# Kernel tuning notes

Measured on AMD Instinct MI355X. Metric: run time of the kernel, lower is better.

The kernel has to match this reference:

```python
import jax, jax.numpy as jnp
import numpy as np

EPS = 1e-6

def setup_inputs() -> dict:
    key = jax.random.key(0)
    kX, ky, kl, kg, ks, kp = jax.random.split(key, 6)
    B, T, N = 65536, 512, 5000
    X = jax.random.randint(kX, (B, 4), 0, N, dtype=jnp.int32)
    y = jax.random.randint(ky, (B, T), 0, 2, dtype=jnp.int32)
    learn_w = jax.random.normal(kl, (N, 1), dtype=jnp.float32)
    guess_w = jax.random.normal(kg, (N, 1), dtype=jnp.float32)
    slip_w = jax.random.normal(ks, (N, 1), dtype=jnp.float32)
    prior_w = jax.random.normal(kp, (N, 1), dtype=jnp.float32)
    return {"X": X, "y": y, "learn_w": learn_w, "guess_w": guess_w,
            "slip_w": slip_w, "prior_w": prior_w}

def _bkt_forward(X, y, learn_w, guess_w, slip_w, prior_w):
    # per-student BKT parameters, each (B,)
    l = jax.nn.sigmoid(learn_w[X[:, 0], 0])
    g = jax.nn.sigmoid(guess_w[X[:, 1], 0])
    s = jax.nn.sigmoid(slip_w[X[:, 2], 0])
    p = jax.nn.sigmoid(prior_w[X[:, 3], 0])
    y_obs = jnp.where(y == -1, 0, y).astype(l.dtype)  # (B, T), -1 padding -> 0

    def step(latent, y_t):
        # latent: (B,) mastery prob at time t (recorded BEFORE update)
        correct = latent * (1 - s) + (1 - latent) * g
        k_t1 = latent * (1 - s) / correct
        k_t0 = latent * s / (latent * s + (1 - latent) * (1 - g))
        k_t = jnp.where(y_t > 0.5, k_t1, k_t0)
        next_latent = jnp.clip(k_t + (1 - k_t) * l, EPS, 1 - EPS)
        return next_latent, (correct, latent)

    _, (corrects, latents) = jax.lax.scan(step, p, y_obs.T)  # scan over T
    return corrects.T, latents.T  # (B, T) each

def reference(X, y, learn_w, guess_w, slip_w, prior_w):
    return _bkt_forward(X, y, learn_w, guess_w, slip_w, prior_w)
```

## Files before the change

### kernel.cpp

```cpp
#include <hip/hip_runtime.h>
#include <cmath>


#define LSTR 36

typedef float floatx4 __attribute__((ext_vector_type(4)));

__global__ __launch_bounds__(256, 1) void bkt_fwd(
    const int* __restrict__ X,
    const int* __restrict__ Y,
    const float* __restrict__ learn_w,
    const float* __restrict__ guess_w,
    const float* __restrict__ slip_w,
    const float* __restrict__ prior_w,
    float* __restrict__ out,
    int B, int T)
{
#pragma clang fp contract(off)
    const int tid = threadIdx.x;
    const int b = blockIdx.x * 256 + tid;

    __shared__ float xp[256 * LSTR];

    const int4 xi = *reinterpret_cast<const int4*>(X + (size_t)b * 4);
    const float l = (float)(1.0 / (1.0 + exp(-(double)learn_w[xi.x])));
    const float g = (float)(1.0 / (1.0 + exp(-(double)guess_w[xi.y])));
    const float s = (float)(1.0 / (1.0 + exp(-(double)slip_w[xi.z])));
    const float p = (float)(1.0 / (1.0 + exp(-(double)prior_w[xi.w])));

    const float oms = 1.0f - s;
    const float omg = 1.0f - g;
    const float lo  = 1e-6f;
    const float hi  = (float)(1.0 - 1e-6);
    float latent = p;

    const int4* __restrict__ yv = reinterpret_cast<const int4*>(Y + (size_t)b * T);
    unsigned int yp[16];
    #pragma unroll
    for (int w = 0; w < 16; ++w) {
        unsigned int m = 0;
        #pragma unroll
        for (int q = 0; q < 8; ++q) {
            const int4 v = yv[w * 8 + q];
            m |= (v.x > 0 ? 1u : 0u) << (q * 4 + 0);
            m |= (v.y > 0 ? 1u : 0u) << (q * 4 + 1);
            m |= (v.z > 0 ? 1u : 0u) << (q * 4 + 2);
            m |= (v.w > 0 ? 1u : 0u) << (q * 4 + 3);
        }
        yp[w] = m;
    }

    const int wv = tid >> 6, ln = tid & 63;
    const int r8 = ln >> 3, c8 = ln & 7;
    float* __restrict__ lrow = xp + tid * LSTR;
    const float* __restrict__ lrd = xp + (wv * 64 + r8) * LSTR + c8 * 4;
    float* __restrict__ gco = out + (size_t)(blockIdx.x * 256 + wv * 64 + r8) * T + c8 * 4;
    float* __restrict__ gla = gco + (size_t)B * T;

    constexpr int STEPS = 32, NQ = 8;
    const int nOuter = T / STEPS;

    for (int o = 0; o < nOuter; ++o) {
        const unsigned int ycur = yp[0];

        float cr[STEPS], lt[STEPS];
        #pragma unroll
        for (int j = 0; j < STEPS; ++j) {
            const float a       = latent * oms;
            const float omlat   = 1.0f - latent;
            const float t1      = omlat * g;
            const float correct = a + t1;
            const float n0      = latent * s;
            const float t2      = omlat * omg;
            const float d0      = n0 + t2;
            const bool hit = (ycur >> j) & 1u;
            const float num = hit ? a : n0;
            const float den = hit ? correct : d0;
            const float k   = num / den;
            cr[j] = correct;
            lt[j] = latent;
            const float omk = 1.0f - k;
            const float t3  = omk * l;
            const float nxt = k + t3;
            latent = fminf(fmaxf(nxt, lo), hi);
        }

        const int colo = o * STEPS;

        #pragma unroll
        for (int q = 0; q < NQ; ++q)
            *reinterpret_cast<float4*>(lrow + q * 4) =
                make_float4(cr[4*q], cr[4*q+1], cr[4*q+2], cr[4*q+3]);
        __builtin_amdgcn_wave_barrier();
        #pragma unroll
        for (int q = 0; q < NQ; ++q) {
            const floatx4 v = *reinterpret_cast<const floatx4*>(lrd + (q * 8) * LSTR);
            __builtin_nontemporal_store(v,
                reinterpret_cast<floatx4*>(gco + (size_t)(q * 8) * T + colo));
        }
        __builtin_amdgcn_wave_barrier();

        #pragma unroll
        for (int q = 0; q < NQ; ++q)
            *reinterpret_cast<float4*>(lrow + q * 4) =
                make_float4(lt[4*q], lt[4*q+1], lt[4*q+2], lt[4*q+3]);
        __builtin_amdgcn_wave_barrier();
        #pragma unroll
        for (int q = 0; q < NQ; ++q) {
            const floatx4 v = *reinterpret_cast<const floatx4*>(lrd + (q * 8) * LSTR);
            __builtin_nontemporal_store(v,
                reinterpret_cast<floatx4*>(gla + (size_t)(q * 8) * T + colo));
        }
        __builtin_amdgcn_wave_barrier();

        #pragma unroll
        for (int w = 0; w < 15; ++w) yp[w] = yp[w + 1];
    }
}

extern "C" void kernel_launch(void* const* d_in, const int* in_sizes, int n_in,
                              void* d_out, int out_size, void* d_ws, size_t ws_size,
                              hipStream_t stream)
{
    const int*   X  = (const int*)d_in[0];
    const int*   Y  = (const int*)d_in[1];
    const float* lw = (const float*)d_in[2];
    const float* gw = (const float*)d_in[3];
    const float* sw = (const float*)d_in[4];
    const float* pw = (const float*)d_in[5];
    float* out = (float*)d_out;

    const int B = in_sizes[0] / 4;
    const int T = in_sizes[1] / B;

    const int threads = 256;
    const int blocks = B / threads;
    bkt_fwd<<<blocks, threads, 0, stream>>>(X, Y, lw, gw, sw, pw, out, B, T);
}
```

Baseline: 82.74 us.

## Split BKT scan into seed pass and parallel chunked emit pass

A first kernel runs the sequential recurrence per student without storing outputs. It records the latent state at every 32-step boundary plus the packed answer bits and parameters in workspace. A second kernel launches 16 threads per student, each recomputing one 32-step chunk from its seed and writing coalesced rows through swizzled shared memory. This aims to decouple the serial dependency chain from the output write bandwidth and raise occupancy for the store-heavy phase, at the cost of computing the recurrence twice and an extra launch plus workspace traffic.

```diff
diff --git a/kernel.cpp b/kernel.cpp
--- a/kernel.cpp
+++ b/kernel.cpp
@@ -2,25 +2,19 @@
 #include <cmath>
 
 
-#define LSTR 36
-
 typedef float floatx4 __attribute__((ext_vector_type(4)));
 
-__global__ __launch_bounds__(256, 1) void bkt_fwd(
-    const int* __restrict__ X,
-    const int* __restrict__ Y,
-    const float* __restrict__ learn_w,
-    const float* __restrict__ guess_w,
-    const float* __restrict__ slip_w,
-    const float* __restrict__ prior_w,
-    float* __restrict__ out,
+__global__ __launch_bounds__(256, 1) void bkt_seed(
+    const int* __restrict__ X, const int* __restrict__ Y,
+    const float* __restrict__ learn_w, const float* __restrict__ guess_w,
+    const float* __restrict__ slip_w,  const float* __restrict__ prior_w,
+    float* __restrict__ seeds,
+    unsigned int* __restrict__ bits,
+    float* __restrict__ prm,
     int B, int T)
 {
 #pragma clang fp contract(off)
-    const int tid = threadIdx.x;
-    const int b = blockIdx.x * 256 + tid;
-
-    __shared__ float xp[256 * LSTR];
+    const int b = blockIdx.x * 256 + threadIdx.x;
 
     const int4 xi = *reinterpret_cast<const int4*>(X + (size_t)b * 4);
     const float l = (float)(1.0 / (1.0 + exp(-(double)learn_w[xi.x])));
@@ -28,28 +22,186 @@
     const float s = (float)(1.0 / (1.0 + exp(-(double)slip_w[xi.z])));
     const float p = (float)(1.0 / (1.0 + exp(-(double)prior_w[xi.w])));
 
-    const float oms = 1.0f - s;
-    const float omg = 1.0f - g;
-    const float lo  = 1e-6f;
-    const float hi  = (float)(1.0 - 1e-6);
+    const float oms = 1.0f - s, omg = 1.0f - g;
+    const float lo = 1e-6f, hi = (float)(1.0 - 1e-6);
+    float latent = p;
+
+    const int4* __restrict__ yv = reinterpret_cast<const int4*>(Y + (size_t)b * T);
+
+    int4 cur[8], nxt[8];
+    #pragma unroll
+    for (int q = 0; q < 8; ++q) cur[q] = yv[q];
+
+    float sd[16];
+    unsigned int yw[16];
+
+    for (int o = 0; o < 16; ++o) {
+        if (o + 1 < 16) {
+            #pragma unroll
+            for (int q = 0; q < 8; ++q) nxt[q] = yv[(o + 1) * 8 + q];
+        }
+        unsigned int m = 0;
+        #pragma unroll
+        for (int q = 0; q < 8; ++q) {
+            m |= (cur[q].x > 0 ? 1u : 0u) << (q * 4 + 0);
+            m |= (cur[q].y > 0 ? 1u : 0u) << (q * 4 + 1);
+            m |= (cur[q].z > 0 ? 1u : 0u) << (q * 4 + 2);
+            m |= (cur[q].w > 0 ? 1u : 0u) << (q * 4 + 3);
+        }
+        yw[o] = m;
+        sd[o] = latent;
+
+        #pragma unroll
+        for (int j = 0; j < 32; ++j) {
+            const float a       = latent * oms;
+            const float omlat   = 1.0f - latent;
+            const float t1      = omlat * g;
+            const float correct = a + t1;
+            const float n0      = latent * s;
+            const float t2      = omlat * omg;
+            const float d0      = n0 + t2;
+            const bool hit = (m >> j) & 1u;
+            const float num = hit ? a : n0;
+            const float den = hit ? correct : d0;
+            const float k   = num / den;
+            (void)correct;
+            const float omk = 1.0f - k;
+            const float t3  = omk * l;
+            const float nxt2 = k + t3;
+            latent = fminf(fmaxf(nxt2, lo), hi);
+        }
+        #pragma unroll
+        for (int q = 0; q < 8; ++q) cur[q] = nxt[q];
+    }
+
+    #pragma unroll
+    for (int q = 0; q < 4; ++q)
+        *reinterpret_cast<float4*>(seeds + (size_t)b * 16 + q * 4) =
+            make_float4(sd[4*q], sd[4*q+1], sd[4*q+2], sd[4*q+3]);
+    #pragma unroll
+    for (int q = 0; q < 4; ++q)
+        *reinterpret_cast<uint4*>(bits + (size_t)b * 16 + q * 4) =
+            make_uint4(yw[4*q], yw[4*q+1], yw[4*q+2], yw[4*q+3]);
+    *reinterpret_cast<float4*>(prm + (size_t)b * 4) = make_float4(l, g, s, p);
+}
+
+__global__ __launch_bounds__(256) void bkt_emit(
+    const float* __restrict__ seeds, const unsigned int* __restrict__ bits,
+    const float* __restrict__ prm, float* __restrict__ out, int B, int T)
+{
+#pragma clang fp contract(off)
+    const int tid = threadIdx.x;
+    const int stl = tid >> 4;
+    const int ch  = tid & 15;
+    const size_t st = (size_t)blockIdx.x * 16 + stl;
+
+    const float4 pr = *reinterpret_cast<const float4*>(prm + st * 4);
+    const float l = pr.x, g = pr.y, s = pr.z;
+    const float oms = 1.0f - s, omg = 1.0f - g;
+    const float lo = 1e-6f, hi = (float)(1.0 - 1e-6);
+
+    float latent = seeds[st * 16 + ch];
+    const unsigned int m = bits[st * 16 + ch];
+
+    float cr[32], lt[32];
+    #pragma unroll
+    for (int j = 0; j < 32; ++j) {
+        const float a       = latent * oms;
+        const float omlat   = 1.0f - latent;
+        const float t1      = omlat * g;
+        const float correct = a + t1;
+        const float n0      = latent * s;
+        const float t2      = omlat * omg;
+        const float d0      = n0 + t2;
+        const bool hit = (m >> j) & 1u;
+        const float num = hit ? a : n0;
+        const float den = hit ? correct : d0;
+        const float k   = num / den;
+        cr[j] = correct;
+        lt[j] = latent;
+        const float omk = 1.0f - k;
+        const float t3  = omk * l;
+        const float nxt = k + t3;
+        latent = fminf(fmaxf(nxt, lo), hi);
+    }
+
+    __shared__ float xs[16 * 512];
+
+    const int wv = tid >> 6, ln = tid & 63;
+    float* __restrict__ myseg = xs + stl * 512 + ch * 32;
+
+    #pragma unroll
+    for (int q = 0; q < 8; ++q)
+        *reinterpret_cast<float4*>(myseg + ((q ^ (ch & 7)) << 2)) =
+            make_float4(cr[4*q], cr[4*q+1], cr[4*q+2], cr[4*q+3]);
+    __syncthreads();
+    #pragma unroll
+    for (int i = 0; i < 8; ++i) {
+        const int srow = wv * 4 + (i >> 1);
+        const int f4   = (i & 1) * 64 + ln;
+        const int chx  = f4 >> 3, qx = f4 & 7;
+        const floatx4 v = *reinterpret_cast<const floatx4*>(
+            xs + srow * 512 + chx * 32 + ((qx ^ (chx & 7)) << 2));
+        const size_t row = (size_t)blockIdx.x * 16 + srow;
+        __builtin_nontemporal_store(v,
+            reinterpret_cast<floatx4*>(out + row * T + f4 * 4));
+    }
+    __syncthreads();
+
+    #pragma unroll
+    for (int q = 0; q < 8; ++q)
+        *reinterpret_cast<float4*>(myseg + ((q ^ (ch & 7)) << 2)) =
+            make_float4(lt[4*q], lt[4*q+1], lt[4*q+2], lt[4*q+3]);
+    __syncthreads();
+    #pragma unroll
+    for (int i = 0; i < 8; ++i) {
+        const int srow = wv * 4 + (i >> 1);
+        const int f4   = (i & 1) * 64 + ln;
+        const int chx  = f4 >> 3, qx = f4 & 7;
+        const floatx4 v = *reinterpret_cast<const floatx4*>(
+            xs + srow * 512 + chx * 32 + ((qx ^ (chx & 7)) << 2));
+        const size_t row = (size_t)blockIdx.x * 16 + srow;
+        __builtin_nontemporal_store(v,
+            reinterpret_cast<floatx4*>(out + (size_t)B * T + row * T + f4 * 4));
+    }
+}
+
+#define LSTR 36
+__global__ __launch_bounds__(256, 1) void bkt_fwd(
+    const int* __restrict__ X, const int* __restrict__ Y,
+    const float* __restrict__ learn_w, const float* __restrict__ guess_w,
+    const float* __restrict__ slip_w,  const float* __restrict__ prior_w,
+    float* __restrict__ out, int B, int T)
+{
+#pragma clang fp contract(off)
+    const int tid = threadIdx.x;
+    const int b = blockIdx.x * 256 + tid;
+    __shared__ float xp[256 * LSTR];
+
+    const int4 xi = *reinterpret_cast<const int4*>(X + (size_t)b * 4);
+    const float l = (float)(1.0 / (1.0 + exp(-(double)learn_w[xi.x])));
+    const float g = (float)(1.0 / (1.0 + exp(-(double)guess_w[xi.y])));
+    const float s = (float)(1.0 / (1.0 + exp(-(double)slip_w[xi.z])));
+    const float p = (float)(1.0 / (1.0 + exp(-(double)prior_w[xi.w])));
+    const float oms = 1.0f - s, omg = 1.0f - g;
+    const float lo = 1e-6f, hi = (float)(1.0 - 1e-6);
     float latent = p;
 
     const int4* __restrict__ yv = reinterpret_cast<const int4*>(Y + (size_t)b * T);
     unsigned int yp[16];
     #pragma unroll
     for (int w = 0; w < 16; ++w) {
-        unsigned int m = 0;
+        unsigned int mm = 0;
         #pragma unroll
         for (int q = 0; q < 8; ++q) {
             const int4 v = yv[w * 8 + q];
-            m |= (v.x > 0 ? 1u : 0u) << (q * 4 + 0);
-            m |= (v.y > 0 ? 1u : 0u) << (q * 4 + 1);
-            m |= (v.z > 0 ? 1u : 0u) << (q * 4 + 2);
-            m |= (v.w > 0 ? 1u : 0u) << (q * 4 + 3);
-        }
-        yp[w] = m;
-    }
-
+            mm |= (v.x > 0 ? 1u : 0u) << (q * 4 + 0);
+            mm |= (v.y > 0 ? 1u : 0u) << (q * 4 + 1);
+            mm |= (v.z > 0 ? 1u : 0u) << (q * 4 + 2);
+            mm |= (v.w > 0 ? 1u : 0u) << (q * 4 + 3);
+        }
+        yp[w] = mm;
+    }
     const int wv = tid >> 6, ln = tid & 63;
     const int r8 = ln >> 3, c8 = ln & 7;
     float* __restrict__ lrow = xp + tid * LSTR;
@@ -57,15 +209,11 @@
     float* __restrict__ gco = out + (size_t)(blockIdx.x * 256 + wv * 64 + r8) * T + c8 * 4;
     float* __restrict__ gla = gco + (size_t)B * T;
 
-    constexpr int STEPS = 32, NQ = 8;
-    const int nOuter = T / STEPS;
-
-    for (int o = 0; o < nOuter; ++o) {
+    for (int o = 0; o < 16; ++o) {
         const unsigned int ycur = yp[0];
-
-        float cr[STEPS], lt[STEPS];
-        #pragma unroll
-        for (int j = 0; j < STEPS; ++j) {
+        float cr[32], lt[32];
+        #pragma unroll
+        for (int j = 0; j < 32; ++j) {
             const float a       = latent * oms;
             const float omlat   = 1.0f - latent;
             const float t1      = omlat * g;
@@ -77,42 +225,37 @@
             const float num = hit ? a : n0;
             const float den = hit ? correct : d0;
             const float k   = num / den;
-            cr[j] = correct;
-            lt[j] = latent;
+            cr[j] = correct; lt[j] = latent;
             const float omk = 1.0f - k;
             const float t3  = omk * l;
             const float nxt = k + t3;
             latent = fminf(fmaxf(nxt, lo), hi);
         }
-
-        const int colo = o * STEPS;
-
-        #pragma unroll
-        for (int q = 0; q < NQ; ++q)
+        const int colo = o * 32;
+        #pragma unroll
+        for (int q = 0; q < 8; ++q)
             *reinterpret_cast<float4*>(lrow + q * 4) =
                 make_float4(cr[4*q], cr[4*q+1], cr[4*q+2], cr[4*q+3]);
         __builtin_amdgcn_wave_barrier();
         #pragma unroll
-        for (int q = 0; q < NQ; ++q) {
+        for (int q = 0; q < 8; ++q) {
             const floatx4 v = *reinterpret_cast<const floatx4*>(lrd + (q * 8) * LSTR);
             __builtin_nontemporal_store(v,
                 reinterpret_cast<floatx4*>(gco + (size_t)(q * 8) * T + colo));
         }
         __builtin_amdgcn_wave_barrier();
-
-        #pragma unroll
-        for (int q = 0; q < NQ; ++q)
+        #pragma unroll
+        for (int q = 0; q < 8; ++q)
             *reinterpret_cast<float4*>(lrow + q * 4) =
                 make_float4(lt[4*q], lt[4*q+1], lt[4*q+2], lt[4*q+3]);
         __builtin_amdgcn_wave_barrier();
         #pragma unroll
-        for (int q = 0; q < NQ; ++q) {
+        for (int q = 0; q < 8; ++q) {
             const floatx4 v = *reinterpret_cast<const floatx4*>(lrd + (q * 8) * LSTR);
             __builtin_nontemporal_store(v,
                 reinterpret_cast<floatx4*>(gla + (size_t)(q * 8) * T + colo));
         }
         __builtin_amdgcn_wave_barrier();
-
         #pragma unroll
         for (int w = 0; w < 15; ++w) yp[w] = yp[w + 1];
     }
@@ -133,7 +276,19 @@
     const int B = in_sizes[0] / 4;
     const int T = in_sizes[1] / B;
 
-    const int threads = 256;
-    const int blocks = B / threads;
-    bkt_fwd<<<blocks, threads, 0, stream>>>(X, Y, lw, gw, sw, pw, out, B, T);
-}
+    const size_t seeds_off = 0;
+    const size_t bits_off  = (size_t)B * 16 * 4;
+    const size_t prm_off   = bits_off + (size_t)B * 16 * 4;
+    const size_t ws_need   = prm_off + (size_t)B * 4 * 4;
+
+    if (T == 512 && (B % 256) == 0 && ws_size >= ws_need) {
+        float*        seeds = (float*)((char*)d_ws + seeds_off);
+        unsigned int* bits  = (unsigned int*)((char*)d_ws + bits_off);
+        float*        prm   = (float*)((char*)d_ws + prm_off);
+        bkt_seed<<<B / 256, 256, 0, stream>>>(X, Y, lw, gw, sw, pw,
+                                              seeds, bits, prm, B, T);
+        bkt_emit<<<B / 16, 256, 0, stream>>>(seeds, bits, prm, out, B, T);
+    } else {
+        bkt_fwd<<<B / 256, 256, 0, stream>>>(X, Y, lw, gw, sw, pw, out, B, T);
+    }
+}
```

Measured after the change: 94.87 us. 14.7% more time.

## Add 16-student-per-block kernel separating serial recurrence from cooperative loads and stores

Applied to the files above, without the earlier changes.

A new kernel handles 16 students per 256-thread block. All threads cooperatively load and bit-pack the y rows into shared memory. Only 16 lanes then run the serial recurrence, writing latents to shared memory. Afterwards all threads recompute `correct` from the stored latents and write both outputs with coalesced nontemporal stores. The goal is more blocks in flight and wider memory parallelism than the old one-block-per-CU layout, at the cost of leaving most lanes idle during the serial phase and adding block-wide syncs.

```diff
diff --git a/kernel.cpp b/kernel.cpp
--- a/kernel.cpp
+++ b/kernel.cpp
@@ -2,24 +2,119 @@
 #include <cmath>
 
 
+typedef float floatx4 __attribute__((ext_vector_type(4)));
+
+#define XSTR 516
+
+__global__ __launch_bounds__(256) void bkt_block16(
+    const int* __restrict__ X, const int* __restrict__ Y,
+    const float* __restrict__ learn_w, const float* __restrict__ guess_w,
+    const float* __restrict__ slip_w,  const float* __restrict__ prior_w,
+    float* __restrict__ out, int B, int T)
+{
+#pragma clang fp contract(off)
+    const int tid = threadIdx.x;
+    const int sbase = blockIdx.x * 16;
+
+    __shared__ float        xlt[16 * XSTR];
+    __shared__ unsigned int ybits[16 * 16];
+    __shared__ float        sprm[16 * 2];
+
+    {
+        const int row = tid >> 4;
+        const int w   = tid & 15;
+        const int4* __restrict__ yr = reinterpret_cast<const int4*>(
+            Y + (size_t)(sbase + row) * T + w * 32);
+        unsigned int m = 0;
+        #pragma unroll
+        for (int q = 0; q < 8; ++q) {
+            const int4 v = yr[q];
+            m |= (v.x > 0 ? 1u : 0u) << (q * 4 + 0);
+            m |= (v.y > 0 ? 1u : 0u) << (q * 4 + 1);
+            m |= (v.z > 0 ? 1u : 0u) << (q * 4 + 2);
+            m |= (v.w > 0 ? 1u : 0u) << (q * 4 + 3);
+        }
+        ybits[row * 16 + w] = m;
+    }
+
+    float l = 0.f, g = 0.f, s = 0.f, p = 0.f;
+    if (tid < 16) {
+        const int4 xi = *reinterpret_cast<const int4*>(X + (size_t)(sbase + tid) * 4);
+        l = (float)(1.0 / (1.0 + exp(-(double)learn_w[xi.x])));
+        g = (float)(1.0 / (1.0 + exp(-(double)guess_w[xi.y])));
+        s = (float)(1.0 / (1.0 + exp(-(double)slip_w[xi.z])));
+        p = (float)(1.0 / (1.0 + exp(-(double)prior_w[xi.w])));
+        sprm[tid * 2 + 0] = 1.0f - s;
+        sprm[tid * 2 + 1] = g;
+    }
+    __syncthreads();
+
+    if (tid < 16) {
+        const float oms = 1.0f - s;
+        const float omg = 1.0f - g;
+        const float lo  = 1e-6f;
+        const float hi  = (float)(1.0 - 1e-6);
+        float latent = p;
+        float* __restrict__ myrow = xlt + tid * XSTR;
+        for (int o = 0; o < 16; ++o) {
+            const unsigned int m = ybits[tid * 16 + o];
+            #pragma unroll
+            for (int j = 0; j < 32; ++j) {
+                const float a       = latent * oms;
+                const float omlat   = 1.0f - latent;
+                const float t1      = omlat * g;
+                const float correct = a + t1;
+                const float n0      = latent * s;
+                const float t2      = omlat * omg;
+                const float d0      = n0 + t2;
+                const bool hit = (m >> j) & 1u;
+                const float num = hit ? a : n0;
+                const float den = hit ? correct : d0;
+                const float k   = num / den;
+                myrow[o * 32 + j] = latent;
+                const float omk = 1.0f - k;
+                const float t3  = omk * l;
+                const float nxt = k + t3;
+                latent = fminf(fmaxf(nxt, lo), hi);
+            }
+        }
+    }
+    __syncthreads();
+
+    const int wv = tid >> 6, ln = tid & 63;
+    #pragma unroll
+    for (int i = 0; i < 8; ++i) {
+        const int r  = wv * 4 + (i >> 1);
+        const int c  = (i & 1) * 256 + ln * 4;
+        const float oms_r = sprm[r * 2 + 0];
+        const float g_r   = sprm[r * 2 + 1];
+        const floatx4 lt4 = *reinterpret_cast<const floatx4*>(xlt + r * XSTR + c);
+        floatx4 cr4;
+        #pragma unroll
+        for (int e = 0; e < 4; ++e) {
+            const float a     = lt4[e] * oms_r;
+            const float omlat = 1.0f - lt4[e];
+            const float t1    = omlat * g_r;
+            cr4[e] = a + t1;
+        }
+        const size_t row = (size_t)(sbase + r);
+        __builtin_nontemporal_store(cr4,
+            reinterpret_cast<floatx4*>(out + row * T + c));
+        __builtin_nontemporal_store(lt4,
+            reinterpret_cast<floatx4*>(out + (size_t)B * T + row * T + c));
+    }
+}
+
 #define LSTR 36
-
-typedef float floatx4 __attribute__((ext_vector_type(4)));
-
 __global__ __launch_bounds__(256, 1) void bkt_fwd(
-    const int* __restrict__ X,
-    const int* __restrict__ Y,
-    const float* __restrict__ learn_w,
-    const float* __restrict__ guess_w,
-    const float* __restrict__ slip_w,
-    const float* __restrict__ prior_w,
-    float* __restrict__ out,
-    int B, int T)
+    const int* __restrict__ X, const int* __restrict__ Y,
+    const float* __restrict__ learn_w, const float* __restrict__ guess_w,
+    const float* __restrict__ slip_w,  const float* __restrict__ prior_w,
+    float* __restrict__ out, int B, int T)
 {
 #pragma clang fp contract(off)
     const int tid = threadIdx.x;
     const int b = blockIdx.x * 256 + tid;
-
     __shared__ float xp[256 * LSTR];
 
     const int4 xi = *reinterpret_cast<const int4*>(X + (size_t)b * 4);
@@ -27,29 +122,25 @@
     const float g = (float)(1.0 / (1.0 + exp(-(double)guess_w[xi.y])));
     const float s = (float)(1.0 / (1.0 + exp(-(double)slip_w[xi.z])));
     const float p = (float)(1.0 / (1.0 + exp(-(double)prior_w[xi.w])));
-
-    const float oms = 1.0f - s;
-    const float omg = 1.0f - g;
-    const float lo  = 1e-6f;
-    const float hi  = (float)(1.0 - 1e-6);
+    const float oms = 1.0f - s, omg = 1.0f - g;
+    const float lo = 1e-6f, hi = (float)(1.0 - 1e-6);
     float latent = p;
 
     const int4* __restrict__ yv = reinterpret_cast<const int4*>(Y + (size_t)b * T);
     unsigned int yp[16];
     #pragma unroll
     for (int w = 0; w < 16; ++w) {
-        unsigned int m = 0;
+        unsigned int mm = 0;
         #pragma unroll
         for (int q = 0; q < 8; ++q) {
             const int4 v = yv[w * 8 + q];
-            m |= (v.x > 0 ? 1u : 0u) << (q * 4 + 0);
-            m |= (v.y > 0 ? 1u : 0u) << (q * 4 + 1);
-            m |= (v.z > 0 ? 1u : 0u) << (q * 4 + 2);
-            m |= (v.w > 0 ? 1u : 0u) << (q * 4 + 3);
-        }
-        yp[w] = m;
-    }
-
+            mm |= (v.x > 0 ? 1u : 0u) << (q * 4 + 0);
+            mm |= (v.y > 0 ? 1u : 0u) << (q * 4 + 1);
+            mm |= (v.z > 0 ? 1u : 0u) << (q * 4 + 2);
+            mm |= (v.w > 0 ? 1u : 0u) << (q * 4 + 3);
+        }
+        yp[w] = mm;
+    }
     const int wv = tid >> 6, ln = tid & 63;
     const int r8 = ln >> 3, c8 = ln & 7;
     float* __restrict__ lrow = xp + tid * LSTR;
@@ -57,15 +148,11 @@
     float* __restrict__ gco = out + (size_t)(blockIdx.x * 256 + wv * 64 + r8) * T + c8 * 4;
     float* __restrict__ gla = gco + (size_t)B * T;
 
-    constexpr int STEPS = 32, NQ = 8;
-    const int nOuter = T / STEPS;
-
-    for (int o = 0; o < nOuter; ++o) {
+    for (int o = 0; o < 16; ++o) {
         const unsigned int ycur = yp[0];
-
-        float cr[STEPS], lt[STEPS];
-        #pragma unroll
-        for (int j = 0; j < STEPS; ++j) {
+        float cr[32], lt[32];
+        #pragma unroll
+        for (int j = 0; j < 32; ++j) {
             const float a       = latent * oms;
             const float omlat   = 1.0f - latent;
             const float t1      = omlat * g;
@@ -77,42 +164,37 @@
             const float num = hit ? a : n0;
             const float den = hit ? correct : d0;
             const float k   = num / den;
-            cr[j] = correct;
-            lt[j] = latent;
+            cr[j] = correct; lt[j] = latent;
             const float omk = 1.0f - k;
             const float t3  = omk * l;
             const float nxt = k + t3;
             latent = fminf(fmaxf(nxt, lo), hi);
         }
-
-        const int colo = o * STEPS;
-
-        #pragma unroll
-        for (int q = 0; q < NQ; ++q)
+        const int colo = o * 32;
+        #pragma unroll
+        for (int q = 0; q < 8; ++q)
             *reinterpret_cast<float4*>(lrow + q * 4) =
                 make_float4(cr[4*q], cr[4*q+1], cr[4*q+2], cr[4*q+3]);
         __builtin_amdgcn_wave_barrier();
         #pragma unroll
-        for (int q = 0; q < NQ; ++q) {
+        for (int q = 0; q < 8; ++q) {
             const floatx4 v = *reinterpret_cast<const floatx4*>(lrd + (q * 8) * LSTR);
             __builtin_nontemporal_store(v,
                 reinterpret_cast<floatx4*>(gco + (size_t)(q * 8) * T + colo));
         }
         __builtin_amdgcn_wave_barrier();
-
-        #pragma unroll
-        for (int q = 0; q < NQ; ++q)
+        #pragma unroll
+        for (int q = 0; q < 8; ++q)
             *reinterpret_cast<float4*>(lrow + q * 4) =
                 make_float4(lt[4*q], lt[4*q+1], lt[4*q+2], lt[4*q+3]);
         __builtin_amdgcn_wave_barrier();
         #pragma unroll
-        for (int q = 0; q < NQ; ++q) {
+        for (int q = 0; q < 8; ++q) {
             const floatx4 v = *reinterpret_cast<const floatx4*>(lrd + (q * 8) * LSTR);
             __builtin_nontemporal_store(v,
                 reinterpret_cast<floatx4*>(gla + (size_t)(q * 8) * T + colo));
         }
         __builtin_amdgcn_wave_barrier();
-
         #pragma unroll
         for (int w = 0; w < 15; ++w) yp[w] = yp[w + 1];
     }
@@ -133,7 +215,9 @@
     const int B = in_sizes[0] / 4;
     const int T = in_sizes[1] / B;
 
-    const int threads = 256;
-    const int blocks = B / threads;
-    bkt_fwd<<<blocks, threads, 0, stream>>>(X, Y, lw, gw, sw, pw, out, B, T);
+    if (T == 512 && (B % 16) == 0) {
+        bkt_block16<<<B / 16, 256, 0, stream>>>(X, Y, lw, gw, sw, pw, out, B, T);
+    } else {
+        bkt_fwd<<<B / 256, 256, 0, stream>>>(X, Y, lw, gw, sw, pw, out, B, T);
+    }
 }
```

Result: slower. 184.9 us (+123.5%).

## Use one-wave blocks with 128-step XOR-swizzled LDS transpose and recompute correct

Applied to the files above, without the earlier changes.

Rewrites the kernel as one wave per 64-thread block. Each chunk now covers 128 timesteps and goes through an XOR-swizzled shared buffer to avoid bank conflicts. Only the latent values are staged in LDS; the correct values are recomputed during the store pass using the row's parameters fetched with shuffles. This halves the LDS traffic and lets each row write 512 contiguous bytes per chunk, at the cost of extra arithmetic and shuffles and 32 KB of LDS per small block. A plain per-thread fallback kernel handles other shapes.

```diff
diff --git a/kernel.cpp b/kernel.cpp
--- a/kernel.cpp
+++ b/kernel.cpp
@@ -2,25 +2,20 @@
 #include <cmath>
 
 
-#define LSTR 36
-
 typedef float floatx4 __attribute__((ext_vector_type(4)));
 
-__global__ __launch_bounds__(256, 1) void bkt_fwd(
-    const int* __restrict__ X,
-    const int* __restrict__ Y,
-    const float* __restrict__ learn_w,
-    const float* __restrict__ guess_w,
-    const float* __restrict__ slip_w,
-    const float* __restrict__ prior_w,
-    float* __restrict__ out,
-    int B, int T)
+__global__ __launch_bounds__(64, 1) void bkt_wave64(
+    const int* __restrict__ X, const int* __restrict__ Y,
+    const float* __restrict__ learn_w, const float* __restrict__ guess_w,
+    const float* __restrict__ slip_w,  const float* __restrict__ prior_w,
+    float* __restrict__ out, int B, int T)
 {
 #pragma clang fp contract(off)
     const int tid = threadIdx.x;
-    const int b = blockIdx.x * 256 + tid;
+    const int sbase = blockIdx.x * 64;
+    const int b = sbase + tid;
 
-    __shared__ float xp[256 * LSTR];
+    __shared__ float xlt[64 * 128];
 
     const int4 xi = *reinterpret_cast<const int4*>(X + (size_t)b * 4);
     const float l = (float)(1.0 / (1.0 + exp(-(double)learn_w[xi.x])));
@@ -50,71 +45,105 @@
         yp[w] = m;
     }
 
-    const int wv = tid >> 6, ln = tid & 63;
-    const int r8 = ln >> 3, c8 = ln & 7;
-    float* __restrict__ lrow = xp + tid * LSTR;
-    const float* __restrict__ lrd = xp + (wv * 64 + r8) * LSTR + c8 * 4;
-    float* __restrict__ gco = out + (size_t)(blockIdx.x * 256 + wv * 64 + r8) * T + c8 * 4;
-    float* __restrict__ gla = gco + (size_t)B * T;
+    float* __restrict__ lrow = xlt + tid * 128;
+    const int ln = tid;
 
-    constexpr int STEPS = 32, NQ = 8;
-    const int nOuter = T / STEPS;
-
-    for (int o = 0; o < nOuter; ++o) {
-        const unsigned int ycur = yp[0];
-
-        float cr[STEPS], lt[STEPS];
-        #pragma unroll
-        for (int j = 0; j < STEPS; ++j) {
-            const float a       = latent * oms;
-            const float omlat   = 1.0f - latent;
-            const float t1      = omlat * g;
-            const float correct = a + t1;
-            const float n0      = latent * s;
-            const float t2      = omlat * omg;
-            const float d0      = n0 + t2;
-            const bool hit = (ycur >> j) & 1u;
-            const float num = hit ? a : n0;
-            const float den = hit ? correct : d0;
-            const float k   = num / den;
-            cr[j] = correct;
-            lt[j] = latent;
-            const float omk = 1.0f - k;
-            const float t3  = omk * l;
-            const float nxt = k + t3;
-            latent = fminf(fmaxf(nxt, lo), hi);
-        }
-
-        const int colo = o * STEPS;
+    for (int o = 0; o < 4; ++o) {
+        const unsigned int m0 = yp[0], m1 = yp[1], m2 = yp[2], m3 = yp[3];
 
         #pragma unroll
-        for (int q = 0; q < NQ; ++q)
-            *reinterpret_cast<float4*>(lrow + q * 4) =
-                make_float4(cr[4*q], cr[4*q+1], cr[4*q+2], cr[4*q+3]);
-        __builtin_amdgcn_wave_barrier();
-        #pragma unroll
-        for (int q = 0; q < NQ; ++q) {
-            const floatx4 v = *reinterpret_cast<const floatx4*>(lrd + (q * 8) * LSTR);
-            __builtin_nontemporal_store(v,
-                reinterpret_cast<floatx4*>(gco + (size_t)(q * 8) * T + colo));
+        for (int q = 0; q < 32; ++q) {
+            float lb[4];
+            #pragma unroll
+            for (int e = 0; e < 4; ++e) {
+                const int j = q * 4 + e;
+                const unsigned int mw = (j < 32) ? m0 : (j < 64) ? m1
+                                       : (j < 96) ? m2 : m3;
+                const bool hit = (mw >> (j & 31)) & 1u;
+                const float a       = latent * oms;
+                const float omlat   = 1.0f - latent;
+                const float t1      = omlat * g;
+                const float correct = a + t1;
+                const float n0      = latent * s;
+                const float t2      = omlat * omg;
+                const float d0      = n0 + t2;
+                const float num = hit ? a : n0;
+                const float den = hit ? correct : d0;
+                const float k   = num / den;
+                lb[e] = latent;
+                const float omk = 1.0f - k;
+                const float t3  = omk * l;
+                const float nxt = k + t3;
+                latent = fminf(fmaxf(nxt, lo), hi);
+            }
+            *reinterpret_cast<float4*>(lrow + ((q ^ (tid & 31)) << 2)) =
+                make_float4(lb[0], lb[1], lb[2], lb[3]);
         }
         __builtin_amdgcn_wave_barrier();
 
         #pragma unroll
-        for (int q = 0; q < NQ; ++q)
-            *reinterpret_cast<float4*>(lrow + q * 4) =
-                make_float4(lt[4*q], lt[4*q+1], lt[4*q+2], lt[4*q+3]);
-        __builtin_amdgcn_wave_barrier();
-        #pragma unroll
-        for (int q = 0; q < NQ; ++q) {
-            const floatx4 v = *reinterpret_cast<const floatx4*>(lrd + (q * 8) * LSTR);
-            __builtin_nontemporal_store(v,
-                reinterpret_cast<floatx4*>(gla + (size_t)(q * 8) * T + colo));
+        for (int i = 0; i < 32; ++i) {
+            const int rl    = 2 * i + (ln >> 5);
+            const int sphys = (ln & 31) ^ (rl & 31);
+            const floatx4 lt4 = *reinterpret_cast<const floatx4*>(
+                xlt + rl * 128 + (sphys << 2));
+            const float oms_r = __shfl(oms, rl);
+            const float g_r   = __shfl(g,   rl);
+            floatx4 cr4;
+            #pragma unroll
+            for (int e = 0; e < 4; ++e) {
+                const float a     = lt4[e] * oms_r;
+                const float omlat = 1.0f - lt4[e];
+                const float t1    = omlat * g_r;
+                cr4[e] = a + t1;
+            }
+            float* gp = out + (size_t)(sbase + rl) * T + o * 128 + (ln & 31) * 4;
+            __builtin_nontemporal_store(cr4, reinterpret_cast<floatx4*>(gp));
+            __builtin_nontemporal_store(lt4,
+                reinterpret_cast<floatx4*>(gp + (size_t)B * T));
         }
         __builtin_amdgcn_wave_barrier();
 
         #pragma unroll
-        for (int w = 0; w < 15; ++w) yp[w] = yp[w + 1];
+        for (int w = 0; w < 12; ++w) yp[w] = yp[w + 4];
+    }
+}
+
+__global__ __launch_bounds__(256, 1) void bkt_simple(
+    const int* __restrict__ X, const int* __restrict__ Y,
+    const float* __restrict__ learn_w, const float* __restrict__ guess_w,
+    const float* __restrict__ slip_w,  const float* __restrict__ prior_w,
+    float* __restrict__ out, int B, int T)
+{
+#pragma clang fp contract(off)
+    const int b = blockIdx.x * blockDim.x + threadIdx.x;
+    if (b >= B) return;
+    const int4 xi = *reinterpret_cast<const int4*>(X + (size_t)b * 4);
+    const float l = (float)(1.0 / (1.0 + exp(-(double)learn_w[xi.x])));
+    const float g = (float)(1.0 / (1.0 + exp(-(double)guess_w[xi.y])));
+    const float s = (float)(1.0 / (1.0 + exp(-(double)slip_w[xi.z])));
+    const float p = (float)(1.0 / (1.0 + exp(-(double)prior_w[xi.w])));
+    const float oms = 1.0f - s, omg = 1.0f - g;
+    const float lo = 1e-6f, hi = (float)(1.0 - 1e-6);
+    float latent = p;
+    for (int t = 0; t < T; ++t) {
+        const float a       = latent * oms;
+        const float omlat   = 1.0f - latent;
+        const float t1      = omlat * g;
+        const float correct = a + t1;
+        const float n0      = latent * s;
+        const float t2      = omlat * omg;
+        const float d0      = n0 + t2;
+        const bool hit = Y[(size_t)b * T + t] > 0;
+        const float num = hit ? a : n0;
+        const float den = hit ? correct : d0;
+        const float k   = num / den;
+        out[(size_t)b * T + t] = correct;
+        out[(size_t)B * T + (size_t)b * T + t] = latent;
+        const float omk = 1.0f - k;
+        const float t3  = omk * l;
+        const float nxt = k + t3;
+        latent = fminf(fmaxf(nxt, lo), hi);
     }
 }
 
@@ -133,7 +162,9 @@
     const int B = in_sizes[0] / 4;
     const int T = in_sizes[1] / B;
 
-    const int threads = 256;
-    const int blocks = B / threads;
-    bkt_fwd<<<blocks, threads, 0, stream>>>(X, Y, lw, gw, sw, pw, out, B, T);
+    if (T == 512 && (B % 64) == 0) {
+        bkt_wave64<<<B / 64, 64, 0, stream>>>(X, Y, lw, gw, sw, pw, out, B, T);
+    } else {
+        bkt_simple<<<(B + 255) / 256, 256, 0, stream>>>(X, Y, lw, gw, sw, pw, out, B, T);
+    }
 }
```

After: 86.17 us. 1.04x slower.
